# Performance work log

Hardware: AMD Instinct MI355X
Metric: run time of the kernel (lower is better)

## Reference

```python
import jax, jax.numpy as jnp
import numpy as np

DIM = 512
H = 8
D = DIM // H  # head_dim = 64
B, N = 2, 2048


def setup_inputs() -> dict:
    key = jax.random.key(0)
    ks = jax.random.split(key, 12)
    s = 1.0 / np.sqrt(DIM)
    inp = {
        "x": jax.random.normal(ks[0], (B, N, DIM), jnp.float32),
        "geo_bias": jax.random.normal(ks[1], (B, H, N, N), jnp.float32),
        "Wq": jax.random.normal(ks[2], (DIM, DIM), jnp.float32) * s,
        "bq": jnp.zeros((DIM,), jnp.float32),
        "Wk": jax.random.normal(ks[3], (DIM, DIM), jnp.float32) * s,
        "bk": jnp.zeros((DIM,), jnp.float32),
        "Wv": jax.random.normal(ks[4], (DIM, DIM), jnp.float32) * s,
        "bv": jnp.zeros((DIM,), jnp.float32),
        "Wo": jax.random.normal(ks[5], (DIM, DIM), jnp.float32) * s,
        "bo": jnp.zeros((DIM,), jnp.float32),
    }
    return inp


def reference(x, geo_bias, Wq, bq, Wk, bk, Wv, bv, Wo, bo):
    # x: (B, N, dim); geo_bias: (B, H, N, N)
    scale = D ** -0.5
    q = (x @ Wq.T + bq).reshape(B, N, H, D)
    k = (x @ Wk.T + bk).reshape(B, N, H, D)
    v = (x @ Wv.T + bv).reshape(B, N, H, D)
    # scores: (B, H, N, N)
    attn = jnp.einsum("bihd,bjhd->bhij", q, k) * scale + geo_bias
    attn = jax.nn.softmax(attn, axis=-1)
    out = jnp.einsum("bhij,bjhd->bihd", attn, v).reshape(B, N, DIM)
    return out @ Wo.T + bo
```

## Files before the change

kernel.cpp:

```cpp
#include <hip/hip_runtime.h>
#include <math.h>

#define SCALE 0.125f

typedef __bf16 bf16;
typedef __bf16 bf16x8 __attribute__((ext_vector_type(8)));
typedef float f32x4 __attribute__((ext_vector_type(4)));

#define WS_XB   0u
#define WS_WB   4194304u
#define WS_Q    6291456u
#define WS_K    10485760u
#define WS_VT   14680064u
#define WS_AT   18874368u

__global__ __launch_bounds__(256) void convert_kernel(
    const float* __restrict__ x, const float* __restrict__ wq,
    const float* __restrict__ wk, const float* __restrict__ wv,
    const float* __restrict__ wo, bf16* __restrict__ xb, bf16* __restrict__ wb) {
  int i = blockIdx.x * 256 + threadIdx.x;
  const float4* src; bf16* dst; int off;
  if (i < 524288) { src = (const float4*)x; dst = xb; off = i; }
  else {
    int j = i - 524288;
    int wsel = j >> 16; off = j & 65535;
    const float* wl = wsel == 0 ? wq : wsel == 1 ? wk : wsel == 2 ? wv : wo;
    src = (const float4*)wl; dst = wb + (wsel << 18);
  }
  float4 v = src[off];
  union { bf16 h[4]; uint2 u; } tmp;
  tmp.h[0] = (bf16)v.x; tmp.h[1] = (bf16)v.y;
  tmp.h[2] = (bf16)v.z; tmp.h[3] = (bf16)v.w;
  ((uint2*)dst)[off] = tmp.u;
}

__global__ __launch_bounds__(256) void qkv_gemm(
    const bf16* __restrict__ xb, const bf16* __restrict__ wb,
    const float* __restrict__ bq, const float* __restrict__ bk,
    const float* __restrict__ bv, bf16* __restrict__ qws,
    bf16* __restrict__ kws, bf16* __restrict__ vtws) {
  __shared__ bf16 Al[128 * 40];
  __shared__ bf16 Bl[64 * 40];
  int t = threadIdx.x;
  int m0 = (blockIdx.x & 31) << 7;
  int n0 = (blockIdx.x >> 5) << 6;
  int lane = t & 63, w = t >> 6;
  int quad = lane >> 4, col = lane & 15;
  int mblk = (w & 1) * 64, nblk = (w >> 1) * 32;
  f32x4 acc[4][2] = {};
  for (int k0 = 0; k0 < 512; k0 += 32) {
    __syncthreads();
    for (int pass = 0; pass < 2; ++pass) {
      int c = t + (pass << 8);
      int row = c >> 2, part = c & 3;
      *(uint4*)&Al[row * 40 + part * 8] =
          *(const uint4*)&xb[(m0 + row) * 512 + k0 + part * 8];
    }
    {
      int row = t >> 2, part = t & 3;
      *(uint4*)&Bl[row * 40 + part * 8] =
          *(const uint4*)&wb[(n0 + row) * 512 + k0 + part * 8];
    }
    __syncthreads();
    bf16x8 af[4], bfv[2];
    for (int i = 0; i < 4; i++)
      af[i] = *(const bf16x8*)&Al[(mblk + i * 16 + col) * 40 + quad * 8];
    for (int i = 0; i < 2; i++)
      bfv[i] = *(const bf16x8*)&Bl[(nblk + i * 16 + col) * 40 + quad * 8];
    for (int mi = 0; mi < 4; mi++)
      for (int ni = 0; ni < 2; ni++)
        acc[mi][ni] = __builtin_amdgcn_mfma_f32_16x16x32_bf16(
            af[mi], bfv[ni], acc[mi][ni], 0, 0, 0);
  }
  for (int mi = 0; mi < 4; mi++)
    for (int ni = 0; ni < 2; ni++) {
      int n = n0 + nblk + ni * 16 + col;
      int wid = n >> 9, feat = n & 511;
      float bias = wid == 0 ? bq[feat] : wid == 1 ? bk[feat] : bv[feat];
      int h = feat >> 6, d = feat & 63;
      int mbase = m0 + mblk + mi * 16 + quad * 4;
      int bidx = mbase >> 11, seq0 = mbase & 2047;
      if (wid == 2) {
        union { bf16 h4[4]; ushort4 u4; } pk;
        for (int r = 0; r < 4; r++) pk.h4[r] = (bf16)(acc[mi][ni][r] + bias);
        *(ushort4*)&vtws[(size_t)((((bidx << 3) + h) << 6) + d) * 2048 + seq0] = pk.u4;
      } else {
        bf16* dst = wid == 0 ? qws : kws;
        for (int r = 0; r < 4; r++)
          dst[(size_t)((((bidx << 3) + h) << 11) + seq0 + r) * 64 + d] =
              (bf16)(acc[mi][ni][r] + bias);
      }
    }
}

__global__ __launch_bounds__(64, 2) void attn_kernel(
    const bf16* __restrict__ qws, const bf16* __restrict__ kws,
    const bf16* __restrict__ vtws, const float* __restrict__ gbias,
    bf16* __restrict__ attn) {
  __shared__ bf16 Pl[16 * 72];
  int lane = threadIdx.x;
  int quad = lane >> 4, col = lane & 15;
  int bid = blockIdx.x;
  int bh = bid >> 7, qt = bid & 127;
  int q0 = qt << 4;
  const bf16* qbase = qws + (size_t)bh * 2048 * 64;
  const bf16* kbase = kws + (size_t)bh * 2048 * 64;
  const bf16* vbase = vtws + (size_t)bh * 64 * 2048;
  const float* bb = gbias + ((size_t)bh * 2048 + q0) * 2048;

  bf16x8 aq[2];
#pragma unroll
  for (int ks = 0; ks < 2; ++ks)
    aq[ks] = *(const bf16x8*)&qbase[(q0 + col) * 64 + ks * 32 + quad * 8];

  f32x4 o[4] = {};
  float mrow[4], lrow[4];
#pragma unroll
  for (int r = 0; r < 4; r++) { mrow[r] = -INFINITY; lrow[r] = 0.f; }

  bf16x8 k2[2][8];
  float bc[2][16];
#pragma unroll
  for (int nt = 0; nt < 4; ++nt)
#pragma unroll
    for (int ks = 0; ks < 2; ++ks)
      k2[0][nt * 2 + ks] =
          *(const bf16x8*)&kbase[(nt * 16 + col) * 64 + ks * 32 + quad * 8];
#pragma unroll
  for (int r = 0; r < 4; r++)
#pragma unroll
    for (int nt = 0; nt < 4; nt++) {
      const float* brow = bb + (size_t)(quad * 4 + r) * 2048;
      bc[0][r * 4 + nt] = brow[nt * 16 + col];
      bc[1][r * 4 + nt] = brow[64 + nt * 16 + col];
    }

  for (int kt = 0; kt < 32; kt += 2) {
#pragma unroll
    for (int u = 0; u < 2; ++u) {
      const int cur = u, nxt = 1 - u;
      int kt_ = kt + u;
      int s0 = kt_ << 6;

      bf16x8 vr[8];
#pragma unroll
      for (int ks = 0; ks < 2; ++ks)
#pragma unroll
        for (int dt = 0; dt < 4; ++dt)
          vr[ks * 4 + dt] = *(const bf16x8*)&vbase[
              (size_t)(dt * 16 + col) * 2048 + s0 + ks * 32 + quad * 8];

      if (kt_ < 31) {
        int s1 = s0 + 64;
#pragma unroll
        for (int nt = 0; nt < 4; ++nt)
#pragma unroll
          for (int ks = 0; ks < 2; ++ks)
            k2[nxt][nt * 2 + ks] = *(const bf16x8*)&kbase[
                (s1 + nt * 16 + col) * 64 + ks * 32 + quad * 8];
      }

      f32x4 s[4];
#pragma unroll
      for (int nt = 0; nt < 4; ++nt) {
        f32x4 a = {};
        a = __builtin_amdgcn_mfma_f32_16x16x32_bf16(aq[0], k2[cur][nt * 2], a, 0, 0, 0);
        a = __builtin_amdgcn_mfma_f32_16x16x32_bf16(aq[1], k2[cur][nt * 2 + 1], a, 0, 0, 0);
        s[nt] = a;
      }

#pragma unroll
      for (int r = 0; r < 4; r++) {
        float sv[4];
        float mx = -INFINITY;
#pragma unroll
        for (int nt = 0; nt < 4; nt++) {
          sv[nt] = s[nt][r] * SCALE + bc[cur][r * 4 + nt];
          mx = fmaxf(mx, sv[nt]);
        }
#pragma unroll
        for (int d = 1; d < 16; d <<= 1) mx = fmaxf(mx, __shfl_xor(mx, d));
        float mnew = fmaxf(mrow[r], mx);
        float alpha = __expf(mrow[r] - mnew);
        float sum = 0.f;
#pragma unroll
        for (int nt = 0; nt < 4; nt++) {
          float e = __expf(sv[nt] - mnew);
          s[nt][r] = e; sum += e;
        }
#pragma unroll
        for (int d = 1; d < 16; d <<= 1) sum += __shfl_xor(sum, d);
        lrow[r] = lrow[r] * alpha + sum;
        mrow[r] = mnew;
#pragma unroll
        for (int dt = 0; dt < 4; ++dt) o[dt][r] *= alpha;
      }

      if (kt_ < 30) {
        int sb = (kt_ + 2) << 6;
#pragma unroll
        for (int r = 0; r < 4; r++) {
          const float* brow = bb + (size_t)(quad * 4 + r) * 2048 + sb;
#pragma unroll
          for (int nt = 0; nt < 4; nt++)
            bc[cur][r * 4 + nt] = brow[nt * 16 + col];
        }
      }

#pragma unroll
      for (int nt = 0; nt < 4; nt++)
#pragma unroll
        for (int r = 0; r < 4; r++)
          Pl[(quad * 4 + r) * 72 + nt * 16 + col] = (bf16)s[nt][r];

#pragma unroll
      for (int ks = 0; ks < 2; ++ks) {
        bf16x8 ap = *(const bf16x8*)&Pl[col * 72 + ks * 32 + quad * 8];
#pragma unroll
        for (int dt = 0; dt < 4; ++dt)
          o[dt] = __builtin_amdgcn_mfma_f32_16x16x32_bf16(ap, vr[ks * 4 + dt], o[dt], 0, 0, 0);
      }
    }
  }

  bf16* obase = attn + (size_t)(bh >> 3) * 2048 * 512 + (bh & 7) * 64;
#pragma unroll
  for (int r = 0; r < 4; r++) {
    float inv = 1.f / lrow[r];
    int gq = q0 + quad * 4 + r;
#pragma unroll
    for (int dt = 0; dt < 4; ++dt)
      obase[(size_t)gq * 512 + dt * 16 + col] = (bf16)(o[dt][r] * inv);
  }
}

__global__ __launch_bounds__(256) void out_gemm(
    const bf16* __restrict__ ab, const bf16* __restrict__ wob,
    const float* __restrict__ bo, float* __restrict__ out) {
  __shared__ bf16 Al[128 * 40];
  __shared__ bf16 Bl[64 * 40];
  int t = threadIdx.x;
  int m0 = (blockIdx.x & 31) << 7;
  int n0 = (blockIdx.x >> 5) << 6;
  int lane = t & 63, w = t >> 6;
  int quad = lane >> 4, col = lane & 15;
  int mblk = (w & 1) * 64, nblk = (w >> 1) * 32;
  f32x4 acc[4][2] = {};
  for (int k0 = 0; k0 < 512; k0 += 32) {
    __syncthreads();
    for (int pass = 0; pass < 2; ++pass) {
      int c = t + (pass << 8);
      int row = c >> 2, part = c & 3;
      *(uint4*)&Al[row * 40 + part * 8] =
          *(const uint4*)&ab[(m0 + row) * 512 + k0 + part * 8];
    }
    {
      int row = t >> 2, part = t & 3;
      *(uint4*)&Bl[row * 40 + part * 8] =
          *(const uint4*)&wob[(n0 + row) * 512 + k0 + part * 8];
    }
    __syncthreads();
    bf16x8 af[4], bfv[2];
    for (int i = 0; i < 4; i++)
      af[i] = *(const bf16x8*)&Al[(mblk + i * 16 + col) * 40 + quad * 8];
    for (int i = 0; i < 2; i++)
      bfv[i] = *(const bf16x8*)&Bl[(nblk + i * 16 + col) * 40 + quad * 8];
    for (int mi = 0; mi < 4; mi++)
      for (int ni = 0; ni < 2; ni++)
        acc[mi][ni] = __builtin_amdgcn_mfma_f32_16x16x32_bf16(
            af[mi], bfv[ni], acc[mi][ni], 0, 0, 0);
  }
  for (int mi = 0; mi < 4; mi++)
    for (int ni = 0; ni < 2; ni++)
      for (int r = 0; r < 4; r++) {
        int m = m0 + mblk + mi * 16 + quad * 4 + r;
        int n = n0 + nblk + ni * 16 + col;
        out[(size_t)m * 512 + n] = acc[mi][ni][r] + bo[n];
      }
}

extern "C" void kernel_launch(void* const* d_in, const int* in_sizes, int n_in,
                              void* d_out, int out_size, void* d_ws, size_t ws_size,
                              hipStream_t stream) {
  const float* x  = (const float*)d_in[0];
  const float* gb = (const float*)d_in[1];
  const float* Wq = (const float*)d_in[2];
  const float* bq = (const float*)d_in[3];
  const float* Wk = (const float*)d_in[4];
  const float* bk = (const float*)d_in[5];
  const float* Wv = (const float*)d_in[6];
  const float* bv = (const float*)d_in[7];
  const float* Wo = (const float*)d_in[8];
  const float* bo = (const float*)d_in[9];
  float* out = (float*)d_out;
  char* ws = (char*)d_ws;
  bf16* xb   = (bf16*)(ws + WS_XB);
  bf16* wb   = (bf16*)(ws + WS_WB);
  bf16* qws  = (bf16*)(ws + WS_Q);
  bf16* kws  = (bf16*)(ws + WS_K);
  bf16* vtws = (bf16*)(ws + WS_VT);
  bf16* at   = (bf16*)(ws + WS_AT);

  hipLaunchKernelGGL(convert_kernel, dim3(3072), dim3(256), 0, stream,
                     x, Wq, Wk, Wv, Wo, xb, wb);
  hipLaunchKernelGGL(qkv_gemm, dim3(768), dim3(256), 0, stream,
                     xb, wb, bq, bk, bv, qws, kws, vtws);
  hipLaunchKernelGGL(attn_kernel, dim3(2048), dim3(64), 0, stream,
                     qws, kws, vtws, gb, at);
  hipLaunchKernelGGL(out_gemm, dim3(256), dim3(256), 0, stream,
                     at, wb + 3 * 262144, bo, out);
}
```

Measured before the change: 488.0 us.

## Split attention key range in two and merge partial softmax results

Each attention block now covers half the keys, which doubles the grid to 4096 single-wave blocks and raises the launch-bounds occupancy hint from 2 to 4. Blocks write unnormalized fp32 partial outputs plus row max and sum to workspace, and a new merge kernel combines the two halves and writes bf16 attention output. The goal is more parallelism and latency hiding for the memory-bound geo_bias stream. The cost is extra global traffic for the fp32 partials, an extra kernel launch, and the loss of K register double-buffering.

```diff
diff --git a/kernel.cpp b/kernel.cpp
--- a/kernel.cpp
+++ b/kernel.cpp
@@ -13,6 +13,8 @@
 #define WS_K    10485760u
 #define WS_VT   14680064u
 #define WS_AT   18874368u
+#define WS_PO   23068672u
+#define WS_ML   39845888u
 
 __global__ __launch_bounds__(256) void convert_kernel(
     const float* __restrict__ x, const float* __restrict__ wq,
@@ -93,20 +95,21 @@
     }
 }
 
-__global__ __launch_bounds__(64, 2) void attn_kernel(
+__global__ __launch_bounds__(64, 4) void attn_kernel(
     const bf16* __restrict__ qws, const bf16* __restrict__ kws,
     const bf16* __restrict__ vtws, const float* __restrict__ gbias,
-    bf16* __restrict__ attn) {
+    float* __restrict__ po, float* __restrict__ ml) {
   __shared__ bf16 Pl[16 * 72];
   int lane = threadIdx.x;
   int quad = lane >> 4, col = lane & 15;
   int bid = blockIdx.x;
-  int bh = bid >> 7, qt = bid & 127;
+  int bh = bid >> 8, qt = (bid >> 1) & 127, kh = bid & 1;
   int q0 = qt << 4;
+  int koff = kh << 10;
   const bf16* qbase = qws + (size_t)bh * 2048 * 64;
-  const bf16* kbase = kws + (size_t)bh * 2048 * 64;
-  const bf16* vbase = vtws + (size_t)bh * 64 * 2048;
-  const float* bb = gbias + ((size_t)bh * 2048 + q0) * 2048;
+  const bf16* kbase = kws + ((size_t)bh * 2048 + koff) * 64;
+  const bf16* vbase = vtws + (size_t)bh * 64 * 2048 + koff;
+  const float* bb = gbias + ((size_t)bh * 2048 + q0) * 2048 + koff;
 
   bf16x8 aq[2];
 #pragma unroll
@@ -118,14 +121,7 @@
 #pragma unroll
   for (int r = 0; r < 4; r++) { mrow[r] = -INFINITY; lrow[r] = 0.f; }
 
-  bf16x8 k2[2][8];
   float bc[2][16];
-#pragma unroll
-  for (int nt = 0; nt < 4; ++nt)
-#pragma unroll
-    for (int ks = 0; ks < 2; ++ks)
-      k2[0][nt * 2 + ks] =
-          *(const bf16x8*)&kbase[(nt * 16 + col) * 64 + ks * 32 + quad * 8];
 #pragma unroll
   for (int r = 0; r < 4; r++)
 #pragma unroll
@@ -135,14 +131,20 @@
       bc[1][r * 4 + nt] = brow[64 + nt * 16 + col];
     }
 
-  for (int kt = 0; kt < 32; kt += 2) {
+  for (int kt = 0; kt < 16; kt += 2) {
 #pragma unroll
     for (int u = 0; u < 2; ++u) {
-      const int cur = u, nxt = 1 - u;
+      const int cur = u;
       int kt_ = kt + u;
       int s0 = kt_ << 6;
 
-      bf16x8 vr[8];
+      bf16x8 kf[8], vr[8];
+#pragma unroll
+      for (int nt = 0; nt < 4; ++nt)
+#pragma unroll
+        for (int ks = 0; ks < 2; ++ks)
+          kf[nt * 2 + ks] = *(const bf16x8*)&kbase[
+              (s0 + nt * 16 + col) * 64 + ks * 32 + quad * 8];
 #pragma unroll
       for (int ks = 0; ks < 2; ++ks)
 #pragma unroll
@@ -150,22 +152,12 @@
           vr[ks * 4 + dt] = *(const bf16x8*)&vbase[
               (size_t)(dt * 16 + col) * 2048 + s0 + ks * 32 + quad * 8];
 
-      if (kt_ < 31) {
-        int s1 = s0 + 64;
-#pragma unroll
-        for (int nt = 0; nt < 4; ++nt)
-#pragma unroll
-          for (int ks = 0; ks < 2; ++ks)
-            k2[nxt][nt * 2 + ks] = *(const bf16x8*)&kbase[
-                (s1 + nt * 16 + col) * 64 + ks * 32 + quad * 8];
-      }
-
       f32x4 s[4];
 #pragma unroll
       for (int nt = 0; nt < 4; ++nt) {
         f32x4 a = {};
-        a = __builtin_amdgcn_mfma_f32_16x16x32_bf16(aq[0], k2[cur][nt * 2], a, 0, 0, 0);
-        a = __builtin_amdgcn_mfma_f32_16x16x32_bf16(aq[1], k2[cur][nt * 2 + 1], a, 0, 0, 0);
+        a = __builtin_amdgcn_mfma_f32_16x16x32_bf16(aq[0], kf[nt * 2], a, 0, 0, 0);
+        a = __builtin_amdgcn_mfma_f32_16x16x32_bf16(aq[1], kf[nt * 2 + 1], a, 0, 0, 0);
         s[nt] = a;
       }
 
@@ -196,7 +188,7 @@
         for (int dt = 0; dt < 4; ++dt) o[dt][r] *= alpha;
       }
 
-      if (kt_ < 30) {
+      if (kt_ < 14) {
         int sb = (kt_ + 2) << 6;
 #pragma unroll
         for (int r = 0; r < 4; r++) {
@@ -223,15 +215,39 @@
     }
   }
 
-  bf16* obase = attn + (size_t)(bh >> 3) * 2048 * 512 + (bh & 7) * 64;
+  size_t rbase = (size_t)(kh * 16 + bh) * 2048 + q0;
 #pragma unroll
   for (int r = 0; r < 4; r++) {
-    float inv = 1.f / lrow[r];
-    int gq = q0 + quad * 4 + r;
+    size_t row = rbase + quad * 4 + r;
 #pragma unroll
     for (int dt = 0; dt < 4; ++dt)
-      obase[(size_t)gq * 512 + dt * 16 + col] = (bf16)(o[dt][r] * inv);
-  }
+      po[row * 64 + dt * 16 + col] = o[dt][r];
+    if (col == 0) {
+      ml[row * 2] = mrow[r];
+      ml[row * 2 + 1] = lrow[r];
+    }
+  }
+}
+
+__global__ __launch_bounds__(256) void merge_kernel(
+    const float* __restrict__ po, const float* __restrict__ ml,
+    bf16* __restrict__ attn) {
+  int i = blockIdx.x * 256 + threadIdx.x;
+  int row = i >> 4, c4 = i & 15;
+  float m1 = ml[row * 2], l1 = ml[row * 2 + 1];
+  float m2 = ml[65536 + row * 2], l2 = ml[65536 + row * 2 + 1];
+  float m = fmaxf(m1, m2);
+  float e1 = __expf(m1 - m), e2 = __expf(m2 - m);
+  float inv = 1.f / (l1 * e1 + l2 * e2);
+  float4 a = *(const float4*)&po[(size_t)row * 64 + c4 * 4];
+  float4 b = *(const float4*)&po[2097152 + (size_t)row * 64 + c4 * 4];
+  union { bf16 h[4]; ushort4 u; } pk;
+  pk.h[0] = (bf16)((a.x * e1 + b.x * e2) * inv);
+  pk.h[1] = (bf16)((a.y * e1 + b.y * e2) * inv);
+  pk.h[2] = (bf16)((a.z * e1 + b.z * e2) * inv);
+  pk.h[3] = (bf16)((a.w * e1 + b.w * e2) * inv);
+  int bh = row >> 11, n = row & 2047;
+  *(ushort4*)&attn[((size_t)(bh >> 3) * 2048 + n) * 512 + (bh & 7) * 64 + c4 * 4] = pk.u;
 }
 
 __global__ __launch_bounds__(256) void out_gemm(
@@ -300,13 +316,17 @@
   bf16* kws  = (bf16*)(ws + WS_K);
   bf16* vtws = (bf16*)(ws + WS_VT);
   bf16* at   = (bf16*)(ws + WS_AT);
+  float* po  = (float*)(ws + WS_PO);
+  float* ml  = (float*)(ws + WS_ML);
 
   hipLaunchKernelGGL(convert_kernel, dim3(3072), dim3(256), 0, stream,
                      x, Wq, Wk, Wv, Wo, xb, wb);
   hipLaunchKernelGGL(qkv_gemm, dim3(768), dim3(256), 0, stream,
                      xb, wb, bq, bk, bv, qws, kws, vtws);
-  hipLaunchKernelGGL(attn_kernel, dim3(2048), dim3(64), 0, stream,
-                     qws, kws, vtws, gb, at);
+  hipLaunchKernelGGL(attn_kernel, dim3(4096), dim3(64), 0, stream,
+                     qws, kws, vtws, gb, po, ml);
+  hipLaunchKernelGGL(merge_kernel, dim3(2048), dim3(256), 0, stream,
+                     po, ml, at);
   hipLaunchKernelGGL(out_gemm, dim3(256), dim3(256), 0, stream,
                      at, wb + 3 * 262144, bo, out);
 }
```

New measurement: 745.4 us. 1.53x slower.
